# Kernel optimization log

Hardware: AMD Instinct MI355X
Metric: run time of the kernel (lower is better)

## Reference

```python
import jax, jax.numpy as jnp
import numpy as np

B, C, W, F, NC = 512, 12, 4, 512, 4  # batch, leads, windows(=4, hardcoded by conv0), features, classes


def setup_inputs() -> dict:
    key = jax.random.key(0)
    ks = jax.random.split(key, 16)
    g = lambda i, shape, s=1.0: jax.random.normal(ks[i], shape, jnp.float32) * s
    return {
        "x": g(0, (B, C, W, F)),
        # GRU (PyTorch layout: W_ih [3F,F], W_hh [3F,F], gate order r,z,n)
        "gru_wih": g(1, (3 * F, F), 0.03),
        "gru_whh": g(2, (3 * F, F), 0.03),
        "gru_bih": jnp.zeros((3 * F,), jnp.float32),
        "gru_bhh": jnp.zeros((3 * F,), jnp.float32),
        # GraphLearning 1x1 convs (squeezed kernels); positive biases keep adj nondegenerate
        "conv0_w": g(3, (W,), 0.5), "conv0_b": jnp.float32(0.1),
        "conv1_w": g(4, (F,), 0.05), "conv1_b": jnp.float32(0.1),
        "conv2_w": g(5, (C * C, C), 0.3),
        "conv2_b": 0.1 + 0.05 * jnp.abs(g(6, (C * C,))),
        # GCN stack
        "gcn_w": g(7, (2, F, F), 0.04), "gcn_b": jnp.zeros((2, F), jnp.float32),
        # classifier head (jax [in,out] layout); BN in eval mode
        "fc1_w": g(8, (C * F, 512), 0.02), "fc1_b": jnp.zeros((512,), jnp.float32),
        "bn1_g": jnp.ones((512,), jnp.float32), "bn1_b": jnp.zeros((512,), jnp.float32),
        "bn1_m": 0.1 * g(9, (512,)), "bn1_v": 1.0 + 0.1 * jnp.abs(g(10, (512,))),
        "fc2_w": g(11, (512, 512), 0.04), "fc2_b": jnp.zeros((512,), jnp.float32),
        "bn2_g": jnp.ones((512,), jnp.float32), "bn2_b": jnp.zeros((512,), jnp.float32),
        "bn2_m": 0.1 * g(12, (512,)), "bn2_v": 1.0 + 0.1 * jnp.abs(g(13, (512,))),
        "fc3_w": g(14, (512, NC), 0.04), "fc3_b": jnp.zeros((NC,), jnp.float32),
    }


def reference(x, gru_wih, gru_whh, gru_bih, gru_bhh,
              conv0_w, conv0_b, conv1_w, conv1_b, conv2_w, conv2_b,
              gcn_w, gcn_b,
              fc1_w, fc1_b, bn1_g, bn1_b, bn1_m, bn1_v,
              fc2_w, fc2_b, bn2_g, bn2_b, bn2_m, bn2_v,
              fc3_w, fc3_b):
    b, c, w, f = x.shape
    # --- GRU over leads dim; each window slice starts from h0=0, so merge (batch, w) ---
    xs = x.transpose(0, 2, 1, 3).reshape(b * w, c, f)            # [N, C, F]
    xW = jnp.einsum('ntf,gf->ntg', xs, gru_wih) + gru_bih        # precompute input gates [N,C,3F]

    def step(h, xw_t):
        hg = h @ gru_whh.T + gru_bhh
        xr, xz, xn = jnp.split(xw_t, 3, axis=-1)
        hr, hz, hn = jnp.split(hg, 3, axis=-1)
        r = jax.nn.sigmoid(xr + hr)
        z = jax.nn.sigmoid(xz + hz)
        n = jnp.tanh(xn + r * hn)
        h = (1.0 - z) * n + z * h
        return h, h

    _, hs = jax.lax.scan(step, jnp.zeros((b * w, f), x.dtype), xW.transpose(1, 0, 2))
    gru_out = hs.transpose(1, 0, 2).reshape(b, w, c, f).transpose(0, 2, 1, 3)  # [B,C,W,F]

    # --- GraphLearning: 1x1 convs -> 12x12 adjacency -> normalized Laplacian -> Chebyshev K=4 ---
    g0 = gru_out.transpose(0, 2, 1, 3)                               # [B,W,C,F]
    y = jax.nn.relu(jnp.einsum('bwcf,w->bcf', g0, conv0_w) + conv0_b)  # [B,C,F]
    y = jax.nn.relu(jnp.einsum('bcf,f->bc', y, conv1_w) + conv1_b)     # [B,C]
    y = jax.nn.relu(jnp.einsum('bc,kc->bk', y, conv2_w) + conv2_b)     # [B,C*C]
    a = jnp.mean(y.reshape(b, c, c), axis=0)
    adj = jax.nn.relu(a)
    degree = jnp.sum(adj, axis=1)
    adj_s = 0.5 * (adj + adj.T)
    d_hat = 1.0 / (jnp.sqrt(degree) + 1e-7)
    lap = d_hat[:, None] * (jnp.diag(degree) - adj_s) * d_hat[None, :]
    L0 = jnp.zeros_like(lap)
    L1 = lap
    L2 = 2.0 * lap @ L1 - L0
    L3 = 2.0 * lap @ L2 - L1
    cheb = jnp.stack([L0, L1, L2, L3], axis=0)                       # [4,C,C]

    # --- GCN stack with residuals (dropout is identity in eval) ---
    h = gru_out.transpose(0, 2, 1, 3)[:, :, None]                    # [B,W,1,C,F]
    tmp = h
    res = h
    for i in range(gcn_w.shape[0]):
        support = jnp.einsum('bwocf,fg->bwocg', h, gcn_w[i])
        out = jnp.einsum('wij,bwojf->bwoif', cheb, support) + gcn_b[i]
        h = jax.nn.relu(out) + res
        res = h
    h = tmp + h
    h = h[:, :, 0].sum(1).reshape(b, c * f)                          # [B, C*F]

    # --- classifier head (eval-mode BN, dropout identity) ---
    def bn(v, gmm, bt, m, var):
        return (v - m) / jnp.sqrt(var + 1e-5) * gmm + bt

    h = bn(jax.nn.leaky_relu(h @ fc1_w + fc1_b, 0.01), bn1_g, bn1_b, bn1_m, bn1_v)
    h = bn(jax.nn.leaky_relu(h @ fc2_w + fc2_b, 0.01), bn2_g, bn2_b, bn2_m, bn2_v)
    return h @ fc3_w + fc3_b
```

## Files before the change

kernel.cpp:

```cpp
#include <hip/hip_runtime.h>
#include <cmath>

constexpr int Bb  = 512;
constexpr int Cc  = 12;
constexpr int Ww  = 4;
constexpr int Ff  = 512;
constexpr int Nn  = Bb * Ww;
constexpr int Gg  = 3 * Ff;
constexpr int Mx  = Nn * Cc;

typedef __attribute__((ext_vector_type(8))) short bf16x8;
typedef __attribute__((ext_vector_type(4))) float f32x4;

__device__ __forceinline__ float sigm(float v) { return 1.f / (1.f + expf(-v)); }
__device__ __forceinline__ float b2f(ushort u) { union { float f; unsigned i; } v; v.i = ((unsigned)u) << 16; return v.f; }
__device__ __forceinline__ ushort f2b(float f) {
    union { float f; unsigned i; } v; v.f = f;
    unsigned r = v.i + 0x7FFFu + ((v.i >> 16) & 1u);
    return (ushort)(r >> 16);
}
__device__ __forceinline__ void async16(const ushort* g, ushort* l) {
    __builtin_amdgcn_global_load_lds(
        (const __attribute__((address_space(1))) unsigned int*)g,
        (__attribute__((address_space(3))) unsigned int*)l, 16, 0, 0);
}

__global__ __launch_bounds__(256) void mfma_gemm(
    const ushort* __restrict__ A, const ushort* __restrict__ Bt,
    float* __restrict__ Cf, ushort* __restrict__ Cb,
    const float* __restrict__ colBias,
    int N, int K, int kLen, int MN, int gridY)
{
    __shared__ ushort As[128 * 64], Bs[128 * 64];
    const int tid = threadIdx.x;
    const int ln = tid & 63, wv = tid >> 6;
    const int l = blockIdx.x;
    const int by = l % gridY, bx = l / gridY, bz = blockIdx.y;
    const int srow = ln >> 3;
    const int kslot = (ln & 7) ^ srow;
    const int rowA0 = by * 128 + wv * 32;
    const int rowB0 = bx * 128 + wv * 32;
    const ushort* ga = A  + (long)(rowA0 + srow) * K + bz * kLen + kslot * 8;
    const ushort* gb = Bt + (long)(rowB0 + srow) * K + bz * kLen + kslot * 8;
    ushort* la = As + wv * 32 * 64;
    ushort* lb = Bs + wv * 32 * 64;
    const int rbase = (wv >> 1) * 64, cbase = (wv & 1) * 64;
    const int mrow = ln & 15, quad = ln >> 4;

    f32x4 acc[4][4] = {};

    for (int kc = 0; kc < kLen; kc += 64) {
        #pragma unroll
        for (int i = 0; i < 4; ++i) {
            async16(ga + (long)(i * 8) * K, la + i * 8 * 64);
            async16(gb + (long)(i * 8) * K, lb + i * 8 * 64);
        }
        ga += 64; gb += 64;
        __syncthreads();
        #pragma unroll
        for (int s = 0; s < 2; ++s) {
            const int sw = (((s << 2) + quad) ^ (ln & 7)) << 3;
            bf16x8 af[4], bf[4];
            #pragma unroll
            for (int i = 0; i < 4; ++i)
                af[i] = *(const bf16x8*)(As + (rbase + i * 16 + mrow) * 64 + sw);
            #pragma unroll
            for (int j = 0; j < 4; ++j)
                bf[j] = *(const bf16x8*)(Bs + (cbase + j * 16 + mrow) * 64 + sw);
            #pragma unroll
            for (int i = 0; i < 4; ++i)
                #pragma unroll
                for (int j = 0; j < 4; ++j)
                    acc[i][j] = __builtin_amdgcn_mfma_f32_16x16x32_bf16(bf[j], af[i], acc[i][j], 0, 0, 0);
        }
        __syncthreads();
    }

    const int gr0 = by * 128 + rbase + mrow;
    const int gc0 = bx * 128 + cbase + quad * 4;
    if (Cb) {
        #pragma unroll
        for (int i = 0; i < 4; ++i) {
            const long rowoff = (long)(gr0 + i * 16) * N;
            #pragma unroll
            for (int j = 0; j < 4; ++j) {
                float c0 = 0.f, c1 = 0.f, c2 = 0.f, c3 = 0.f;
                if (colBias) {
                    const float4 cb4 = *(const float4*)(colBias + gc0 + j * 16);
                    c0 = cb4.x; c1 = cb4.y; c2 = cb4.z; c3 = cb4.w;
                }
                union { ushort u[4]; uint2 v; } pk;
                pk.u[0] = f2b(acc[i][j][0] + c0);
                pk.u[1] = f2b(acc[i][j][1] + c1);
                pk.u[2] = f2b(acc[i][j][2] + c2);
                pk.u[3] = f2b(acc[i][j][3] + c3);
                *(uint2*)&Cb[rowoff + gc0 + j * 16] = pk.v;
            }
        }
    } else {
        float* Co = Cf + (long)bz * MN;
        #pragma unroll
        for (int i = 0; i < 4; ++i) {
            const long rowoff = (long)(gr0 + i * 16) * N;
            #pragma unroll
            for (int j = 0; j < 4; ++j)
                *(f32x4*)&Co[rowoff + gc0 + j * 16] = acc[i][j];
        }
    }
}

__global__ __launch_bounds__(256) void gru_fused(
    const ushort* __restrict__ hin, const ushort* __restrict__ xb,
    const ushort* __restrict__ whhB, const ushort* __restrict__ wihB,
    const float* __restrict__ bih, const float* __restrict__ bhh,
    ushort* __restrict__ hout, ushort* __restrict__ G, int t)
{
    __shared__ ushort Ah[64 * 64], Ax[64 * 64], Bh[96 * 64], Bx[96 * 64];
    const int tid = threadIdx.x, ln = tid & 63, wv = tid >> 6;
    const int mb = blockIdx.x & 31, fb = blockIdx.x >> 5;
    const int srow = ln >> 3, kslot = (ln & 7) ^ srow;
    const int mrow = ln & 15, quad = ln >> 4;
    f32x4 aH[6] = {}, aX[6] = {};
    const ushort* hrow = hin + (long)(mb * 64) * 512;

    for (int kc = 0; kc < 512; kc += 64) {
        #pragma unroll
        for (int a = 0; a < 2; ++a) {
            const int r0 = (wv * 2 + a) * 8;
            async16(hrow + (long)(r0 + srow) * 512 + kc + kslot * 8, Ah + r0 * 64);
            async16(xb + ((long)(mb * 64 + r0 + srow) * 12 + t) * 512 + kc + kslot * 8, Ax + r0 * 64);
        }
        #pragma unroll
        for (int b8 = 0; b8 < 3; ++b8) {
            const int lr0 = (wv * 3 + b8) * 8;
            const int lr = lr0 + srow;
            const int g = lr >> 5, fc = lr & 31;
            const long wr = (long)(g * 512 + fb * 32 + fc) * 512 + kc + kslot * 8;
            async16(whhB + wr, Bh + lr0 * 64);
            async16(wihB + wr, Bx + lr0 * 64);
        }
        __syncthreads();
        #pragma unroll
        for (int s = 0; s < 2; ++s) {
            const int sw = (((s << 2) + quad) ^ (ln & 7)) << 3;
            const bf16x8 ah = *(const bf16x8*)(Ah + (wv * 16 + mrow) * 64 + sw);
            const bf16x8 ax = *(const bf16x8*)(Ax + (wv * 16 + mrow) * 64 + sw);
            #pragma unroll
            for (int jt = 0; jt < 6; ++jt) {
                const bf16x8 bh = *(const bf16x8*)(Bh + (jt * 16 + mrow) * 64 + sw);
                aH[jt] = __builtin_amdgcn_mfma_f32_16x16x32_bf16(bh, ah, aH[jt], 0, 0, 0);
            }
            #pragma unroll
            for (int jt = 0; jt < 6; ++jt) {
                const bf16x8 bx2 = *(const bf16x8*)(Bx + (jt * 16 + mrow) * 64 + sw);
                aX[jt] = __builtin_amdgcn_mfma_f32_16x16x32_bf16(bx2, ax, aX[jt], 0, 0, 0);
            }
        }
        __syncthreads();
    }

    const int n = mb * 64 + wv * 16 + mrow;
    #pragma unroll
    for (int ft = 0; ft < 2; ++ft) {
        const int f0 = fb * 32 + ft * 16 + quad * 4;
        const float4 bir = *(const float4*)(bih + f0);
        const float4 biz = *(const float4*)(bih + 512 + f0);
        const float4 bin = *(const float4*)(bih + 1024 + f0);
        const float4 bhr = *(const float4*)(bhh + f0);
        const float4 bhz = *(const float4*)(bhh + 512 + f0);
        const float4 bhn = *(const float4*)(bhh + 1024 + f0);
        union { ushort u[4]; uint2 v; } hp;
        hp.v = *(const uint2*)(hin + (long)n * 512 + f0);
        const float br[4] = {bir.x + bhr.x, bir.y + bhr.y, bir.z + bhr.z, bir.w + bhr.w};
        const float bz[4] = {biz.x + bhz.x, biz.y + bhz.y, biz.z + bhz.z, biz.w + bhz.w};
        const float bn_i[4] = {bin.x, bin.y, bin.z, bin.w};
        const float bn_h[4] = {bhn.x, bhn.y, bhn.z, bhn.w};
        union { ushort u[4]; uint2 v; } o;
        #pragma unroll
        for (int r = 0; r < 4; ++r) {
            const float rr = sigm(aH[ft][r] + aX[ft][r] + br[r]);
            const float zz = sigm(aH[2 + ft][r] + aX[2 + ft][r] + bz[r]);
            const float nv = tanhf(aX[4 + ft][r] + bn_i[r] + rr * (aH[4 + ft][r] + bn_h[r]));
            o.u[r] = f2b((1.f - zz) * nv + zz * b2f(hp.u[r]));
        }
        *(uint2*)&hout[(long)n * 512 + f0] = o.v;
        *(uint2*)&G[(long)(n * 12 + t) * 512 + f0] = o.v;
    }
}

__global__ __launch_bounds__(256) void cvt_x(const float* __restrict__ x, ushort* __restrict__ xb)
{
    const int idx = blockIdx.x * 256 + threadIdx.x;
    const int m = idx >> 6, f8 = (idx & 63) << 3;
    const int n = m / 12, c = m - n * 12;
    const int b = n >> 2, w = n & 3;
    const float* src = x + (((b * 12 + c) * 4 + w) << 9) + f8;
    const float4 a = *(const float4*)src, q = *(const float4*)(src + 4);
    uint4 o;
    o.x = (unsigned)f2b(a.x) | ((unsigned)f2b(a.y) << 16);
    o.y = (unsigned)f2b(a.z) | ((unsigned)f2b(a.w) << 16);
    o.z = (unsigned)f2b(q.x) | ((unsigned)f2b(q.y) << 16);
    o.w = (unsigned)f2b(q.z) | ((unsigned)f2b(q.w) << 16);
    *(uint4*)(xb + (m << 9) + f8) = o;
}

__global__ __launch_bounds__(256) void cvt_w2(
    const float* __restrict__ wih, const float* __restrict__ whh,
    ushort* __restrict__ wihB, ushort* __restrict__ whhB)
{
    int bx = blockIdx.x;
    const float* s; ushort* d;
    if (bx < 384) { s = wih; d = wihB; } else { s = whh; d = whhB; bx -= 384; }
    const int e = (bx * 256 + threadIdx.x) << 3;
    const float4 a = *(const float4*)(s + e), q = *(const float4*)(s + e + 4);
    uint4 o;
    o.x = (unsigned)f2b(a.x) | ((unsigned)f2b(a.y) << 16);
    o.y = (unsigned)f2b(a.z) | ((unsigned)f2b(a.w) << 16);
    o.z = (unsigned)f2b(q.x) | ((unsigned)f2b(q.y) << 16);
    o.w = (unsigned)f2b(q.z) | ((unsigned)f2b(q.w) << 16);
    *(uint4*)(d + e) = o;
}

__global__ __launch_bounds__(256) void tcvt_all(
    const float* __restrict__ gcnw, const float* __restrict__ f1w, const float* __restrict__ f2w,
    ushort* __restrict__ gw0, ushort* __restrict__ gw1,
    ushort* __restrict__ f1t, ushort* __restrict__ f2t)
{
    int by = blockIdx.y;
    const float* src; ushort* dst; int R, C;
    if (by < 16)       { src = gcnw;          dst = gw0; R = 512;  C = 512; }
    else if (by < 32)  { src = gcnw + 262144; dst = gw1; R = 512;  C = 512; by -= 16; }
    else if (by < 224) { src = f1w;           dst = f1t; R = 6144; C = 512; by -= 32; }
    else               { src = f2w;           dst = f2t; R = 512;  C = 512; by -= 224; }
    __shared__ float tl[32][33];
    const int c0 = blockIdx.x * 32, r0 = by * 32;
    const int cx = threadIdx.x & 31, ry = threadIdx.x >> 5;
    #pragma unroll
    for (int k = 0; k < 4; ++k) tl[ry + k * 8][cx] = src[(long)(r0 + ry + k * 8) * C + c0 + cx];
    __syncthreads();
    #pragma unroll
    for (int k = 0; k < 4; ++k) dst[(long)(c0 + ry + k * 8) * R + r0 + cx] = f2b(tl[cx][ry + k * 8]);
}

__global__ __launch_bounds__(256) void conv01(
    const ushort* __restrict__ G, const float* __restrict__ w0, const float* __restrict__ b0,
    const float* __restrict__ w1, const float* __restrict__ b1, float* __restrict__ y2)
{
    const int row = (blockIdx.x * 256 + threadIdx.x) >> 6;
    const int lane = threadIdx.x & 63;
    const int b = row / 12, c = row - 12 * b;
    const float w00 = w0[0], w01 = w0[1], w02 = w0[2], w03 = w0[3], bb = b0[0];
    const ushort* gp = G + ((long)(b * 4) * 12 + c) * 512;
    float s = 0.f;
    for (int f = lane; f < 512; f += 64) {
        const float v = bb + b2f(gp[f]) * w00 + b2f(gp[6144 + f]) * w01
                      + b2f(gp[12288 + f]) * w02 + b2f(gp[18432 + f]) * w03;
        s += fmaxf(v, 0.f) * w1[f];
    }
    #pragma unroll
    for (int off = 32; off; off >>= 1) s += __shfl_down(s, off);
    if (lane == 0) y2[row] = fmaxf(s + b1[0], 0.f);
}

__global__ __launch_bounds__(256) void conv2_cheb(
    const float* __restrict__ y2, const float* __restrict__ w2,
    const float* __restrict__ b2, float* __restrict__ cheb)
{
    __shared__ float ys[6144];
    __shared__ float adj[144], deg[12], dhat[12], lap[144], T2[144];
    const int tid = threadIdx.x;
    for (int i = tid; i < 6144; i += 256) ys[i] = y2[i];
    __syncthreads();
    if (tid < 144) {
        float wk[12];
        #pragma unroll
        for (int c = 0; c < 12; ++c) wk[c] = w2[tid * 12 + c];
        const float bias = b2[tid];
        float s = 0.f;
        for (int b = 0; b < 512; ++b) {
            float v = bias;
            #pragma unroll
            for (int c = 0; c < 12; ++c) v += ys[b * 12 + c] * wk[c];
            s += fmaxf(v, 0.f);
        }
        adj[tid] = fmaxf(s * (1.f / 512.f), 0.f);
    }
    __syncthreads();
    if (tid < 12) {
        float s = 0.f;
        for (int j = 0; j < 12; ++j) s += adj[tid * 12 + j];
        deg[tid] = s; dhat[tid] = 1.f / (sqrtf(s) + 1e-7f);
    }
    __syncthreads();
    if (tid < 144) {
        const int i = tid / 12, j = tid % 12;
        const float as = 0.5f * (adj[i * 12 + j] + adj[j * 12 + i]);
        lap[tid] = dhat[i] * ((i == j ? deg[i] : 0.f) - as) * dhat[j];
    }
    __syncthreads();
    if (tid < 144) {
        const int i = tid / 12, j = tid % 12;
        float s = 0.f;
        for (int kk = 0; kk < 12; ++kk) s += lap[i * 12 + kk] * lap[kk * 12 + j];
        T2[tid] = 2.f * s;
    }
    __syncthreads();
    if (tid < 144) {
        const int i = tid / 12, j = tid % 12;
        float s = 0.f;
        for (int kk = 0; kk < 12; ++kk) s += lap[i * 12 + kk] * T2[kk * 12 + j];
        cheb[tid] = 0.f;
        cheb[144 + tid] = lap[tid];
        cheb[288 + tid] = T2[tid];
        cheb[432 + tid] = 2.f * s - lap[tid];
    }
}

__global__ __launch_bounds__(256) void gcn_epi1(
    const ushort* __restrict__ S, const float* __restrict__ cheb,
    const float* __restrict__ gcnb, const ushort* __restrict__ G,
    ushort* __restrict__ H1)
{
    __shared__ float ch[576];
    const int tid = threadIdx.x;
    for (int i = tid; i < 576; i += 256) ch[i] = cheb[i];
    __syncthreads();
    const int idx = blockIdx.x * 256 + tid;
    const int f = idx & 511, bc = idx >> 9;
    const int b = bc / 12, c = bc - 12 * b;
    const float bias = gcnb[f];
    #pragma unroll
    for (int w = 0; w < 4; ++w) {
        float o = bias;
        const ushort* Sr = S + ((b * 4 + w) * 12) * 512 + f;
        const float* cw = ch + w * 144 + c * 12;
        #pragma unroll
        for (int j = 0; j < 12; ++j) o += cw[j] * b2f(Sr[j * 512]);
        const int gi = ((b * 4 + w) * 12 + c) * 512 + f;
        H1[gi] = f2b(fmaxf(o, 0.f) + b2f(G[gi]));
    }
}

__global__ __launch_bounds__(256) void gcn_epi2(
    const ushort* __restrict__ S, const float* __restrict__ cheb,
    const float* __restrict__ gcnb, const ushort* __restrict__ G,
    const ushort* __restrict__ H1, ushort* __restrict__ pooled)
{
    __shared__ float ch[576];
    const int tid = threadIdx.x;
    for (int i = tid; i < 576; i += 256) ch[i] = cheb[i];
    __syncthreads();
    const int idx = blockIdx.x * 256 + tid;
    const int f = idx & 511, bc = idx >> 9;
    const int b = bc / 12, c = bc - 12 * b;
    const float bias = gcnb[f];
    float acc = 0.f;
    #pragma unroll
    for (int w = 0; w < 4; ++w) {
        float o = bias;
        const ushort* Sr = S + ((b * 4 + w) * 12) * 512 + f;
        const float* cw = ch + w * 144 + c * 12;
        #pragma unroll
        for (int j = 0; j < 12; ++j) o += cw[j] * b2f(Sr[j * 512]);
        const int gi = ((b * 4 + w) * 12 + c) * 512 + f;
        acc += fmaxf(o, 0.f) + b2f(H1[gi]) + b2f(G[gi]);
    }
    pooled[idx] = f2b(acc);
}

__global__ __launch_bounds__(256) void fc_epi(
    const float* __restrict__ part, int nsplit, const float* __restrict__ bias,
    const float* __restrict__ g, const float* __restrict__ be,
    const float* __restrict__ mu, const float* __restrict__ var,
    ushort* __restrict__ outb, float* __restrict__ outf)
{
    const int idx = blockIdx.x * 256 + threadIdx.x;
    const int c = idx & 511;
    float s = bias[c];
    for (int k = 0; k < nsplit; ++k) s += part[k * 262144 + idx];
    s = s >= 0.f ? s : 0.01f * s;
    s = (s - mu[c]) * rsqrtf(var[c] + 1e-5f) * g[c] + be[c];
    if (outb) outb[idx] = f2b(s); else outf[idx] = s;
}

__global__ __launch_bounds__(256) void fc3_kernel(
    const float* __restrict__ z2, const float* __restrict__ w3,
    const float* __restrict__ b3, float* __restrict__ out)
{
    const int idx = blockIdx.x * 256 + threadIdx.x;
    const int m = idx >> 2, nc = idx & 3;
    float s = b3[nc];
    const float* zr = z2 + m * 512;
    for (int k = 0; k < 512; ++k) s += zr[k] * w3[k * 4 + nc];
    out[idx] = s;
}

extern "C" void kernel_launch(void* const* d_in, const int* in_sizes, int n_in,
                              void* d_out, int out_size, void* d_ws, size_t ws_size,
                              hipStream_t stream)
{
    (void)in_sizes; (void)n_in; (void)out_size; (void)ws_size;
    const float* x    = (const float*)d_in[0];
    const float* wih  = (const float*)d_in[1];
    const float* whh  = (const float*)d_in[2];
    const float* bih  = (const float*)d_in[3];
    const float* bhh  = (const float*)d_in[4];
    const float* c0w  = (const float*)d_in[5];
    const float* c0b  = (const float*)d_in[6];
    const float* c1w  = (const float*)d_in[7];
    const float* c1b  = (const float*)d_in[8];
    const float* c2w  = (const float*)d_in[9];
    const float* c2b  = (const float*)d_in[10];
    const float* gcnw = (const float*)d_in[11];
    const float* gcnb = (const float*)d_in[12];
    const float* f1w  = (const float*)d_in[13];
    const float* f1b  = (const float*)d_in[14];
    const float* bn1g = (const float*)d_in[15];
    const float* bn1b = (const float*)d_in[16];
    const float* bn1m = (const float*)d_in[17];
    const float* bn1v = (const float*)d_in[18];
    const float* f2w  = (const float*)d_in[19];
    const float* f2b_ = (const float*)d_in[20];
    const float* bn2g = (const float*)d_in[21];
    const float* bn2b = (const float*)d_in[22];
    const float* bn2m = (const float*)d_in[23];
    const float* bn2v = (const float*)d_in[24];
    const float* f3w  = (const float*)d_in[25];
    const float* f3b  = (const float*)d_in[26];

    char* W = (char*)d_ws;
    ushort* xb     = (ushort*)(W + 0);
    ushort* pooled = (ushort*)(W + 0);
    float*  z1p    = (float*)(W + 8388608);
    float*  z2p    = z1p;
    ushort* G      = (ushort*)(W + 25165824);
    ushort* S      = (ushort*)(W + 50331648);
    ushort* H1     = (ushort*)(W + 75497472);
    ushort* h0     = (ushort*)(W + 100663296);
    ushort* h1     = (ushort*)(W + 102760448);
    ushort* wihB   = (ushort*)(W + 104857600);
    ushort* whhB   = (ushort*)(W + 106430464);
    ushort* gw0    = (ushort*)(W + 108003328);
    ushort* gw1    = (ushort*)(W + 108527616);
    ushort* f1t    = (ushort*)(W + 109051904);
    ushort* f2t    = (ushort*)(W + 115343360);
    ushort* z1b    = (ushort*)(W + 115867648);
    float*  z2     = (float*)(W + 116391936);
    float*  y2     = (float*)(W + 117440512);
    float*  chebb  = (float*)(W + 117465088);

    hipMemsetAsync(h0, 0, (size_t)Nn * Ff * sizeof(ushort), stream);
    cvt_x<<<(Mx * 64) / 256, 256, 0, stream>>>(x, xb);
    cvt_w2<<<768, 256, 0, stream>>>(wih, whh, wihB, whhB);
    tcvt_all<<<dim3(16, 240), 256, 0, stream>>>(gcnw, f1w, f2w, gw0, gw1, f1t, f2t);

    ushort* hp = h0; ushort* hq = h1;
    for (int t = 0; t < Cc; ++t) {
        gru_fused<<<512, 256, 0, stream>>>(hp, xb, whhB, wihB, bih, bhh, hq, G, t);
        ushort* tmp = hp; hp = hq; hq = tmp;
    }

    conv01<<<(Bb * Cc * 64) / 256, 256, 0, stream>>>(G, c0w, c0b, c1w, c1b, y2);
    conv2_cheb<<<1, 256, 0, stream>>>(y2, c2w, c2b, chebb);

    mfma_gemm<<<dim3(768, 1), 256, 0, stream>>>(
        G, gw0, nullptr, S, nullptr, Ff, Ff, Ff, 0, 192);
    gcn_epi1<<<(Bb * Cc * Ff) / 256, 256, 0, stream>>>(S, chebb, gcnb, G, H1);

    mfma_gemm<<<dim3(768, 1), 256, 0, stream>>>(
        H1, gw1, nullptr, S, nullptr, Ff, Ff, Ff, 0, 192);
    gcn_epi2<<<(Bb * Cc * Ff) / 256, 256, 0, stream>>>(S, chebb, gcnb + Ff, G, H1, pooled);

    mfma_gemm<<<dim3(16, 16), 256, 0, stream>>>(
        pooled, f1t, z1p, nullptr, nullptr, 512, Cc * Ff, 384, 262144, 4);
    fc_epi<<<1024, 256, 0, stream>>>(z1p, 16, f1b, bn1g, bn1b, bn1m, bn1v, z1b, nullptr);
    mfma_gemm<<<dim3(16, 4), 256, 0, stream>>>(
        z1b, f2t, z2p, nullptr, nullptr, 512, 512, 128, 262144, 4);
    fc_epi<<<1024, 256, 0, stream>>>(z2p, 4, f2b_, bn2g, bn2b, bn2m, bn2v, nullptr, z2);
    fc3_kernel<<<(Bb * 4) / 256, 256, 0, stream>>>(z2, f3w, f3b, (float*)d_out);
}
```

Baseline: 493.5 us.

## Fuse GRU timesteps into one persistent kernel with grid barriers

The twelve per-timestep GRU launches become a single persistent kernel of 512 blocks that loops over timesteps. Blocks synchronise between steps through an atomic counter barrier in global memory, and block indices are remapped so blocks sharing weight slices are grouped. Biases are hoisted out of the time loop. conv01 and conv2_cheb are merged with a last-block-done ticket, which removes a launch. This relies on all 512 blocks being co-resident, otherwise the spin barrier deadlocks.

```diff
diff --git a/kernel.cpp b/kernel.cpp
--- a/kernel.cpp
+++ b/kernel.cpp
@@ -109,57 +109,23 @@
     }
 }
 
-__global__ __launch_bounds__(256) void gru_fused(
-    const ushort* __restrict__ hin, const ushort* __restrict__ xb,
+__global__ __launch_bounds__(256) void gru_all(
+    const ushort* __restrict__ xb,
     const ushort* __restrict__ whhB, const ushort* __restrict__ wihB,
     const float* __restrict__ bih, const float* __restrict__ bhh,
-    ushort* __restrict__ hout, ushort* __restrict__ G, int t)
+    ushort* __restrict__ h0, ushort* __restrict__ h1,
+    ushort* __restrict__ G, unsigned* __restrict__ cnt)
 {
     __shared__ ushort Ah[64 * 64], Ax[64 * 64], Bh[96 * 64], Bx[96 * 64];
     const int tid = threadIdx.x, ln = tid & 63, wv = tid >> 6;
-    const int mb = blockIdx.x & 31, fb = blockIdx.x >> 5;
+    const int p = blockIdx.x;
+    const int fb = ((p & 7) << 1) | (p >> 8);
+    const int mb = (p >> 3) & 31;
     const int srow = ln >> 3, kslot = (ln & 7) ^ srow;
     const int mrow = ln & 15, quad = ln >> 4;
-    f32x4 aH[6] = {}, aX[6] = {};
-    const ushort* hrow = hin + (long)(mb * 64) * 512;
-
-    for (int kc = 0; kc < 512; kc += 64) {
-        #pragma unroll
-        for (int a = 0; a < 2; ++a) {
-            const int r0 = (wv * 2 + a) * 8;
-            async16(hrow + (long)(r0 + srow) * 512 + kc + kslot * 8, Ah + r0 * 64);
-            async16(xb + ((long)(mb * 64 + r0 + srow) * 12 + t) * 512 + kc + kslot * 8, Ax + r0 * 64);
-        }
-        #pragma unroll
-        for (int b8 = 0; b8 < 3; ++b8) {
-            const int lr0 = (wv * 3 + b8) * 8;
-            const int lr = lr0 + srow;
-            const int g = lr >> 5, fc = lr & 31;
-            const long wr = (long)(g * 512 + fb * 32 + fc) * 512 + kc + kslot * 8;
-            async16(whhB + wr, Bh + lr0 * 64);
-            async16(wihB + wr, Bx + lr0 * 64);
-        }
-        __syncthreads();
-        #pragma unroll
-        for (int s = 0; s < 2; ++s) {
-            const int sw = (((s << 2) + quad) ^ (ln & 7)) << 3;
-            const bf16x8 ah = *(const bf16x8*)(Ah + (wv * 16 + mrow) * 64 + sw);
-            const bf16x8 ax = *(const bf16x8*)(Ax + (wv * 16 + mrow) * 64 + sw);
-            #pragma unroll
-            for (int jt = 0; jt < 6; ++jt) {
-                const bf16x8 bh = *(const bf16x8*)(Bh + (jt * 16 + mrow) * 64 + sw);
-                aH[jt] = __builtin_amdgcn_mfma_f32_16x16x32_bf16(bh, ah, aH[jt], 0, 0, 0);
-            }
-            #pragma unroll
-            for (int jt = 0; jt < 6; ++jt) {
-                const bf16x8 bx2 = *(const bf16x8*)(Bx + (jt * 16 + mrow) * 64 + sw);
-                aX[jt] = __builtin_amdgcn_mfma_f32_16x16x32_bf16(bx2, ax, aX[jt], 0, 0, 0);
-            }
-        }
-        __syncthreads();
-    }
-
     const int n = mb * 64 + wv * 16 + mrow;
+
+    float br[2][4], bz[2][4], bnI[2][4], bnH[2][4];
     #pragma unroll
     for (int ft = 0; ft < 2; ++ft) {
         const int f0 = fb * 32 + ft * 16 + quad * 4;
@@ -169,22 +135,81 @@
         const float4 bhr = *(const float4*)(bhh + f0);
         const float4 bhz = *(const float4*)(bhh + 512 + f0);
         const float4 bhn = *(const float4*)(bhh + 1024 + f0);
-        union { ushort u[4]; uint2 v; } hp;
-        hp.v = *(const uint2*)(hin + (long)n * 512 + f0);
-        const float br[4] = {bir.x + bhr.x, bir.y + bhr.y, bir.z + bhr.z, bir.w + bhr.w};
-        const float bz[4] = {biz.x + bhz.x, biz.y + bhz.y, biz.z + bhz.z, biz.w + bhz.w};
-        const float bn_i[4] = {bin.x, bin.y, bin.z, bin.w};
-        const float bn_h[4] = {bhn.x, bhn.y, bhn.z, bhn.w};
-        union { ushort u[4]; uint2 v; } o;
-        #pragma unroll
-        for (int r = 0; r < 4; ++r) {
-            const float rr = sigm(aH[ft][r] + aX[ft][r] + br[r]);
-            const float zz = sigm(aH[2 + ft][r] + aX[2 + ft][r] + bz[r]);
-            const float nv = tanhf(aX[4 + ft][r] + bn_i[r] + rr * (aH[4 + ft][r] + bn_h[r]));
-            o.u[r] = f2b((1.f - zz) * nv + zz * b2f(hp.u[r]));
-        }
-        *(uint2*)&hout[(long)n * 512 + f0] = o.v;
-        *(uint2*)&G[(long)(n * 12 + t) * 512 + f0] = o.v;
+        br[ft][0] = bir.x + bhr.x; br[ft][1] = bir.y + bhr.y; br[ft][2] = bir.z + bhr.z; br[ft][3] = bir.w + bhr.w;
+        bz[ft][0] = biz.x + bhz.x; bz[ft][1] = biz.y + bhz.y; bz[ft][2] = biz.z + bhz.z; bz[ft][3] = biz.w + bhz.w;
+        bnI[ft][0] = bin.x; bnI[ft][1] = bin.y; bnI[ft][2] = bin.z; bnI[ft][3] = bin.w;
+        bnH[ft][0] = bhn.x; bnH[ft][1] = bhn.y; bnH[ft][2] = bhn.z; bnH[ft][3] = bhn.w;
+    }
+
+    const ushort* hp = h0;
+    ushort* hq = h1;
+    for (int t = 0; t < Cc; ++t) {
+        f32x4 aH[6] = {}, aX[6] = {};
+        const ushort* hrow = hp + (long)(mb * 64) * 512;
+
+        for (int kc = 0; kc < 512; kc += 64) {
+            #pragma unroll
+            for (int a = 0; a < 2; ++a) {
+                const int r0 = (wv * 2 + a) * 8;
+                async16(hrow + (long)(r0 + srow) * 512 + kc + kslot * 8, Ah + r0 * 64);
+                async16(xb + ((long)(mb * 64 + r0 + srow) * 12 + t) * 512 + kc + kslot * 8, Ax + r0 * 64);
+            }
+            #pragma unroll
+            for (int b8 = 0; b8 < 3; ++b8) {
+                const int lr0 = (wv * 3 + b8) * 8;
+                const int lr = lr0 + srow;
+                const int g = lr >> 5, fc = lr & 31;
+                const long wr = (long)(g * 512 + fb * 32 + fc) * 512 + kc + kslot * 8;
+                async16(whhB + wr, Bh + lr0 * 64);
+                async16(wihB + wr, Bx + lr0 * 64);
+            }
+            __syncthreads();
+            #pragma unroll
+            for (int s = 0; s < 2; ++s) {
+                const int sw = (((s << 2) + quad) ^ (ln & 7)) << 3;
+                const bf16x8 ah = *(const bf16x8*)(Ah + (wv * 16 + mrow) * 64 + sw);
+                const bf16x8 ax = *(const bf16x8*)(Ax + (wv * 16 + mrow) * 64 + sw);
+                #pragma unroll
+                for (int jt = 0; jt < 6; ++jt) {
+                    const bf16x8 bh = *(const bf16x8*)(Bh + (jt * 16 + mrow) * 64 + sw);
+                    aH[jt] = __builtin_amdgcn_mfma_f32_16x16x32_bf16(bh, ah, aH[jt], 0, 0, 0);
+                }
+                #pragma unroll
+                for (int jt = 0; jt < 6; ++jt) {
+                    const bf16x8 bx2 = *(const bf16x8*)(Bx + (jt * 16 + mrow) * 64 + sw);
+                    aX[jt] = __builtin_amdgcn_mfma_f32_16x16x32_bf16(bx2, ax, aX[jt], 0, 0, 0);
+                }
+            }
+            __syncthreads();
+        }
+
+        #pragma unroll
+        for (int ft = 0; ft < 2; ++ft) {
+            const int f0 = fb * 32 + ft * 16 + quad * 4;
+            union { ushort u[4]; uint2 v; } hpk;
+            hpk.v = *(const uint2*)(hp + (long)n * 512 + f0);
+            union { ushort u[4]; uint2 v; } o;
+            #pragma unroll
+            for (int r = 0; r < 4; ++r) {
+                const float rr = sigm(aH[ft][r] + aX[ft][r] + br[ft][r]);
+                const float zz = sigm(aH[2 + ft][r] + aX[2 + ft][r] + bz[ft][r]);
+                const float nv = tanhf(aX[4 + ft][r] + bnI[ft][r] + rr * (aH[4 + ft][r] + bnH[ft][r]));
+                o.u[r] = f2b((1.f - zz) * nv + zz * b2f(hpk.u[r]));
+            }
+            *(uint2*)&hq[(long)n * 512 + f0] = o.v;
+            *(uint2*)&G[(long)(n * 12 + t) * 512 + f0] = o.v;
+        }
+
+        if (t < Cc - 1) {
+            __syncthreads();
+            if (tid == 0) {
+                __hip_atomic_fetch_add(&cnt[t], 1u, __ATOMIC_RELEASE, __HIP_MEMORY_SCOPE_AGENT);
+                while (__hip_atomic_load(&cnt[t], __ATOMIC_ACQUIRE, __HIP_MEMORY_SCOPE_AGENT) < 512u)
+                    __builtin_amdgcn_s_sleep(8);
+            }
+            __syncthreads();
+        }
+        const ushort* tmp = hp; hp = hq; hq = (ushort*)tmp;
     }
 }
 
@@ -242,33 +267,38 @@
     for (int k = 0; k < 4; ++k) dst[(long)(c0 + ry + k * 8) * R + r0 + cx] = f2b(tl[cx][ry + k * 8]);
 }
 
-__global__ __launch_bounds__(256) void conv01(
+__global__ __launch_bounds__(256) void conv01_cheb(
     const ushort* __restrict__ G, const float* __restrict__ w0, const float* __restrict__ b0,
-    const float* __restrict__ w1, const float* __restrict__ b1, float* __restrict__ y2)
-{
-    const int row = (blockIdx.x * 256 + threadIdx.x) >> 6;
-    const int lane = threadIdx.x & 63;
-    const int b = row / 12, c = row - 12 * b;
-    const float w00 = w0[0], w01 = w0[1], w02 = w0[2], w03 = w0[3], bb = b0[0];
-    const ushort* gp = G + ((long)(b * 4) * 12 + c) * 512;
-    float s = 0.f;
-    for (int f = lane; f < 512; f += 64) {
-        const float v = bb + b2f(gp[f]) * w00 + b2f(gp[6144 + f]) * w01
-                      + b2f(gp[12288 + f]) * w02 + b2f(gp[18432 + f]) * w03;
-        s += fmaxf(v, 0.f) * w1[f];
-    }
-    #pragma unroll
-    for (int off = 32; off; off >>= 1) s += __shfl_down(s, off);
-    if (lane == 0) y2[row] = fmaxf(s + b1[0], 0.f);
-}
-
-__global__ __launch_bounds__(256) void conv2_cheb(
-    const float* __restrict__ y2, const float* __restrict__ w2,
-    const float* __restrict__ b2, float* __restrict__ cheb)
-{
+    const float* __restrict__ w1, const float* __restrict__ b1,
+    const float* __restrict__ w2, const float* __restrict__ b2,
+    float* __restrict__ y2, float* __restrict__ cheb, unsigned* __restrict__ done)
+{
+    const int tid = threadIdx.x;
+    {
+        const int row = (blockIdx.x * 256 + tid) >> 6;
+        const int lane = tid & 63;
+        const int b = row / 12, c = row - 12 * b;
+        const float w00 = w0[0], w01 = w0[1], w02 = w0[2], w03 = w0[3], bb = b0[0];
+        const ushort* gp = G + ((long)(b * 4) * 12 + c) * 512;
+        float s = 0.f;
+        for (int f = lane; f < 512; f += 64) {
+            const float v = bb + b2f(gp[f]) * w00 + b2f(gp[6144 + f]) * w01
+                          + b2f(gp[12288 + f]) * w02 + b2f(gp[18432 + f]) * w03;
+            s += fmaxf(v, 0.f) * w1[f];
+        }
+        #pragma unroll
+        for (int off = 32; off; off >>= 1) s += __shfl_down(s, off);
+        if (lane == 0) y2[row] = fmaxf(s + b1[0], 0.f);
+    }
+    __syncthreads();
+    __shared__ unsigned ticket;
+    if (tid == 0)
+        ticket = __hip_atomic_fetch_add(done, 1u, __ATOMIC_ACQ_REL, __HIP_MEMORY_SCOPE_AGENT);
+    __syncthreads();
+    if (ticket != gridDim.x - 1) return;
+
     __shared__ float ys[6144];
     __shared__ float adj[144], deg[12], dhat[12], lap[144], T2[144];
-    const int tid = threadIdx.x;
     for (int i = tid; i < 6144; i += 256) ys[i] = y2[i];
     __syncthreads();
     if (tid < 144) {
@@ -448,20 +478,18 @@
     float*  z2     = (float*)(W + 116391936);
     float*  y2     = (float*)(W + 117440512);
     float*  chebb  = (float*)(W + 117465088);
+    unsigned* sync = (unsigned*)(W + 117469184);
 
     hipMemsetAsync(h0, 0, (size_t)Nn * Ff * sizeof(ushort), stream);
+    hipMemsetAsync(sync, 0, 64, stream);
     cvt_x<<<(Mx * 64) / 256, 256, 0, stream>>>(x, xb);
     cvt_w2<<<768, 256, 0, stream>>>(wih, whh, wihB, whhB);
     tcvt_all<<<dim3(16, 240), 256, 0, stream>>>(gcnw, f1w, f2w, gw0, gw1, f1t, f2t);
 
-    ushort* hp = h0; ushort* hq = h1;
-    for (int t = 0; t < Cc; ++t) {
-        gru_fused<<<512, 256, 0, stream>>>(hp, xb, whhB, wihB, bih, bhh, hq, G, t);
-        ushort* tmp = hp; hp = hq; hq = tmp;
-    }
-
-    conv01<<<(Bb * Cc * 64) / 256, 256, 0, stream>>>(G, c0w, c0b, c1w, c1b, y2);
-    conv2_cheb<<<1, 256, 0, stream>>>(y2, c2w, c2b, chebb);
+    gru_all<<<512, 256, 0, stream>>>(xb, whhB, wihB, bih, bhh, h0, h1, G, sync);
+
+    conv01_cheb<<<(Bb * Cc * 64) / 256, 256, 0, stream>>>(
+        G, c0w, c0b, c1w, c1b, c2w, c2b, y2, chebb, sync + 12);
 
     mfma_gemm<<<dim3(768, 1), 256, 0, stream>>>(
         G, gw0, nullptr, S, nullptr, Ff, Ff, Ff, 0, 192);
```

Result: slower. 1.027 ms (+108.1%).
